# Kernel optimization log

Measured on AMD Instinct MI355X. Metric: run time of the kernel, lower is better.

The kernel has to match this reference:

```python
import math
import jax, jax.numpy as jnp
from jax import lax
import numpy as np

THETA = 10.0      # spiking threshold
TAU_SR = 10.0     # SRM (psp) alpha-kernel time constant
TAU_REF = 1.0     # refractory alpha-kernel time constant
SCALE_REF = 2.0   # refractory scale (kernel = -scaleRef*theta*alpha)
TAU_RHO = 1.0     # surrogate-gradient width
TS = 1.0          # simulation time step


def _alpha_filter_scan(x, tau, extra_input_fn=None):
    """Causal convolution along last (time) axis with alpha kernel
    k[n] = (n*Ts/tau) * exp(1 - n*Ts/tau)  (k[0] = 0),
    implemented exactly as a 2-state linear recurrence.
    x: [N, C, T] -> out: [N, C, T]."""
    d = jnp.float32(math.exp(-TS / tau))
    c = jnp.float32(math.e * TS / tau)
    xT = jnp.moveaxis(x, -1, 0)  # [T, N, C]

    def step(carry, xt):
        p, a = carry
        a = d * (a + p)          # alpha response from inputs up to t-1
        p = d * p + xt           # pure exponential state
        return (p, a), a * c

    z = jnp.zeros_like(xT[0])
    _, out = lax.scan(step, (z, z), xT)
    return jnp.moveaxis(out, 0, -1)


def psp(x):
    return _alpha_filter_scan(x, TAU_SR)


@jax.custom_vjp
def spike_fn(v):
    # Heaviside threshold on (membrane - theta)
    return (v >= 0).astype(v.dtype)

def _spike_fwd(v):
    return spike_fn(v), v

def _spike_bwd(v, g):
    # SLAYER surrogate gradient: exponential pdf around threshold
    grad = (1.0 / TAU_RHO) * jnp.exp(-jnp.abs(v) / TAU_RHO)
    return (g * grad,)

spike_fn.defvjp(_spike_fwd, _spike_bwd)


def spike_layer(u_in):
    """Threshold-and-refract over time. u_in: [N, C, T] psp potentials.
    Refractory response = -scaleRef*theta * alpha_{tauRef}(past spikes)."""
    d = jnp.float32(math.exp(-TS / TAU_REF))
    c = jnp.float32(math.e * TS / TAU_REF)
    ref_scale = jnp.float32(-SCALE_REF * THETA)
    uT = jnp.moveaxis(u_in, -1, 0)  # [T, N, C]

    def step(carry, ut):
        p, a = carry
        a = d * (a + p)                      # refractory potential at t
        u = ut + c * a                       # membrane potential
        s = spike_fn(u - THETA)              # spikes (0/1)
        p = d * p + ref_scale * s            # inject refractory impulse
        return (p, a), s

    z = jnp.zeros_like(uT[0])
    _, s = lax.scan(step, (z, z), uT)
    return jnp.moveaxis(s, 0, -1)


def setup_inputs() -> dict:
    key = jax.random.key(0)
    k1, k2, k3 = jax.random.split(key, 3)
    N, I, H, O, T = 64, 256, 1024, 18, 500
    # Bernoulli(0.1) input spikes
    spike_input = (jax.random.uniform(k1, (N, I, T)) < 0.1).astype(jnp.float32)
    W1 = jax.random.normal(k2, (H, I), dtype=jnp.float32) * (1.0 / math.sqrt(I))
    W2 = jax.random.normal(k3, (O, H), dtype=jnp.float32) * (1.0 / math.sqrt(H))
    return {"spike_input": spike_input, "W1": W1, "W2": W2}


def reference(spike_input, W1, W2):
    # layer 1: dense (per-timestep linear) -> psp -> spike
    y1 = jnp.einsum('nit,hi->nht', spike_input, W1)
    s1 = spike_layer(psp(y1))
    # layer 2
    y2 = jnp.einsum('nht,oh->not', s1, W2)
    s2 = spike_layer(psp(y2))
    return s2
```

## Files before the change

kernel.cpp:

```cpp
#include <hip/hip_runtime.h>


#define NN 64
#define II 256
#define HH 1024
#define OO 18
#define TT 500

#define D_SR 0.9048374180359595f
#define C_SR 0.27182818284590454f
#define D_RF 0.36787944117144233f
#define C_RF 2.718281828459045f
#define THETA 10.0f
#define REFS (-20.0f)

typedef _Float16 f16;
typedef _Float16 f16x8 __attribute__((ext_vector_type(8)));
typedef float f32x4 __attribute__((ext_vector_type(4)));

__device__ __forceinline__ void gl2lds16(const void* g, void* l) {
    __builtin_amdgcn_global_load_lds(
        (const __attribute__((address_space(1))) void*)g,
        (__attribute__((address_space(3))) void*)l, 16, 0, 0);
}

__launch_bounds__(256)
__global__ void prep_all(const float* __restrict__ X, const float* __restrict__ W1,
                         const float* __restrict__ W2, f16* __restrict__ Xb,
                         f16* __restrict__ W1h, f16* __restrict__ W1l,
                         f16* __restrict__ W2h, f16* __restrict__ W2l) {
    __shared__ float tile[64][65];
    const int b = blockIdx.x;
    const int tid = threadIdx.x;

    if (b < 2048) {
        const int t0 = (b & 7) * 64, i0 = ((b >> 3) & 3) * 64, n = b >> 5;
        const int tx = tid & 63, q = tid >> 6;
        const float* Xn = X + (size_t)n * II * TT;
#pragma unroll 4
        for (int j = 0; j < 16; ++j) {
            int il = j * 4 + q;
            int t = t0 + tx;
            tile[il][tx] = (t < TT) ? Xn[(size_t)(i0 + il) * TT + t] : 0.f;
        }
        __syncthreads();
#pragma unroll 4
        for (int j = 0; j < 16; ++j) {
            int tl = j * 4 + q;
            int t = t0 + tl;
            if (t < TT)
                Xb[((size_t)n * TT + t) * II + i0 + tx] = (f16)tile[tx][tl];
        }
    } else if (b < 3072) {
        int idx = (b - 2048) * 256 + tid;
        float w = W1[idx];
        f16 h = (f16)w;
        f16 l = (f16)(w - (float)h);
        W1h[idx] = h;
        W1l[idx] = l;
    } else {
        int idx = (b - 3072) * 256 + tid;
        int o = idx >> 10;
        float w = (o < OO) ? W2[idx] : 0.f;
        f16 h = (f16)w;
        f16 l = (f16)(w - (float)h);
        W2h[idx] = h;
        W2l[idx] = l;
    }
}

__launch_bounds__(512)
__global__ void gemm1_scan1(const f16* __restrict__ Xb, const f16* __restrict__ Wh,
                            const f16* __restrict__ Wl, f16* __restrict__ S1) {
    __shared__ __align__(16) char smem[3 * 24576];
    float* yb = (float*)smem;

    const int tid = threadIdx.x;
    const int wave = tid >> 6, lane = tid & 63;

    const int f = blockIdx.y * 8 + blockIdx.x;
    const int x = f & 7, g = f >> 3;
    const int n = x * 8 + (g & 7);
    const int ht = g >> 3;
    const int h0g = ht * 128;

    const int rbl = wave * 16 + (lane >> 2);
    const int koff = (((lane & 3) ^ ((lane >> 3) & 3))) * 8;
    const f16* gBh0 = Wh + (size_t)(h0g + rbl) * II + koff;
    const f16* gBl0 = Wl + (size_t)(h0g + rbl) * II + koff;

    const int wm = wave & 1, wn = wave >> 1;
    const int fr = lane & 15, kq = lane >> 4;
    const int kz = (kq ^ ((fr >> 1) & 3)) * 8;

    float p1 = 0.f, a1 = 0.f, p2 = 0.f, a2 = 0.f;

    for (int c = 0; c < 4; ++c) {
        const int t0 = c * 128;
        const int TCe = (TT - t0 < 128) ? (TT - t0) : 128;

        int r0 = rbl; if (r0 > TCe - 1) r0 = TCe - 1;
        const f16* gA0 = Xb + ((size_t)n * TT + t0 + r0) * II + koff;

        auto stage = [&](int kk2, int b) {
            f16* As_b = (f16*)(smem + b * 24576);
            f16* Bh_b = As_b + 4096;
            f16* Bl_b = As_b + 8192;
            const int ko = kk2 * 32;
            gl2lds16(gA0 + ko, As_b + wave * 512);
            gl2lds16(gBh0 + ko, Bh_b + wave * 512);
            gl2lds16(gBl0 + ko, Bl_b + wave * 512);
        };

        stage(0, 0);
        stage(1, 1);

        f32x4 acc[4][2] = {};
#pragma unroll
        for (int kk = 0; kk < 8; ++kk) {
            if (kk < 7) asm volatile("s_waitcnt vmcnt(3)" ::: "memory");
            else        asm volatile("s_waitcnt vmcnt(0)" ::: "memory");
            __builtin_amdgcn_s_barrier();
            __builtin_amdgcn_sched_barrier(0);
            if (kk < 6) stage(kk + 2, (kk + 2) % 3);

            const f16* As_b = (const f16*)(smem + (kk % 3) * 24576);
            const f16* Bh_b = As_b + 4096;
            const f16* Bl_b = As_b + 8192;

            f16x8 av[4], bhv[2], blv[2];
#pragma unroll
            for (int i = 0; i < 4; ++i)
                av[i] = *(const f16x8*)(As_b + (wm * 64 + i * 16 + fr) * 32 + kz);
#pragma unroll
            for (int j = 0; j < 2; ++j) {
                bhv[j] = *(const f16x8*)(Bh_b + (wn * 32 + j * 16 + fr) * 32 + kz);
                blv[j] = *(const f16x8*)(Bl_b + (wn * 32 + j * 16 + fr) * 32 + kz);
            }
            __builtin_amdgcn_s_setprio(1);
#pragma unroll
            for (int i = 0; i < 4; ++i)
#pragma unroll
                for (int j = 0; j < 2; ++j) {
                    acc[i][j] = __builtin_amdgcn_mfma_f32_16x16x32_f16(av[i], bhv[j], acc[i][j], 0, 0, 0);
                    acc[i][j] = __builtin_amdgcn_mfma_f32_16x16x32_f16(av[i], blv[j], acc[i][j], 0, 0, 0);
                }
            __builtin_amdgcn_s_setprio(0);
        }
        __syncthreads();

#pragma unroll
        for (int i = 0; i < 4; ++i)
#pragma unroll
            for (int j = 0; j < 2; ++j) {
                int tr = wm * 64 + i * 16 + kq * 4;
                int hc = wn * 32 + j * 16 + fr;
#pragma unroll
                for (int r = 0; r < 4; ++r)
                    yb[(tr + r) * 132 + hc] = acc[i][j][r];
            }
        __syncthreads();

        if (tid < 128) {
            f16* sq = S1 + ((size_t)n * TT + t0) * HH + h0g + tid;
            float rb_[8];
#pragma unroll
            for (int j = 0; j < 8; ++j) rb_[j] = yb[j * 132 + tid];
            int t = 0;
            for (; t + 8 <= TCe; t += 8) {
#pragma unroll
                for (int j = 0; j < 8; ++j) {
                    float xv = rb_[j];
                    int tn = t + j + 8;
                    rb_[j] = (tn < TCe) ? yb[tn * 132 + tid] : 0.f;
                    a1 = D_SR * (a1 + p1);
                    p1 = D_SR * p1 + xv;
                    float ut = C_SR * a1;
                    a2 = D_RF * (a2 + p2);
                    float u = ut + C_RF * a2;
                    float s = (u >= THETA) ? 1.0f : 0.0f;
                    p2 = D_RF * p2 + REFS * s;
                    sq[(size_t)(t + j) * HH] = (f16)s;
                }
            }
            int rem = TCe - t;
#pragma unroll
            for (int j = 0; j < 8; ++j) {
                if (j < rem) {
                    float xv = rb_[j];
                    a1 = D_SR * (a1 + p1);
                    p1 = D_SR * p1 + xv;
                    float ut = C_SR * a1;
                    a2 = D_RF * (a2 + p2);
                    float u = ut + C_RF * a2;
                    float s = (u >= THETA) ? 1.0f : 0.0f;
                    p2 = D_RF * p2 + REFS * s;
                    sq[(size_t)(t + j) * HH] = (f16)s;
                }
            }
        }
        __syncthreads();
    }
}

__launch_bounds__(256)
__global__ void gemm2_mfma(const f16* __restrict__ S1, const f16* __restrict__ W2h,
                           const f16* __restrict__ W2l, float* __restrict__ Y2) {
    __shared__ __align__(16) f16 As[3][64 * 32];
    __shared__ __align__(16) f16 Bh[3][32 * 32];
    __shared__ __align__(16) f16 Bl[3][32 * 32];

    const int tid = threadIdx.x;
    const int wave = tid >> 6, lane = tid & 63;
    const int m0 = blockIdx.x * 64;
    const int fr = lane & 15, kq = lane >> 4;
    const int koff = (((lane & 3) ^ ((lane >> 3) & 3))) * 8;
    const int kz = (kq ^ ((fr >> 1) & 3)) * 8;

    const f16* gA = S1 + (size_t)(m0 + wave * 16 + (lane >> 2)) * HH + koff;
    const f16* gB = (wave < 2 ? W2h : W2l) + (size_t)((wave & 1) * 16 + (lane >> 2)) * HH + koff;

    auto stage = [&](int kk2, int b) {
        const int ko = kk2 * 32;
        gl2lds16(gA + ko, &As[b][wave * 512]);
        gl2lds16(gB + ko, (wave < 2 ? &Bh[b][0] : &Bl[b][0]) + (wave & 1) * 512);
    };

    stage(0, 0);
    stage(1, 1);

    f32x4 acc[2] = {};
#pragma unroll
    for (int kk = 0; kk < HH / 32; ++kk) {
        if (kk < HH / 32 - 1) asm volatile("s_waitcnt vmcnt(2)" ::: "memory");
        else                  asm volatile("s_waitcnt vmcnt(0)" ::: "memory");
        __builtin_amdgcn_s_barrier();
        __builtin_amdgcn_sched_barrier(0);
        if (kk < HH / 32 - 2) stage(kk + 2, (kk + 2) % 3);
        const int b = kk % 3;

        f16x8 a, bh[2], bl[2];
        a = *(const f16x8*)(&As[b][(wave * 16 + fr) * 32 + kz]);
#pragma unroll
        for (int j = 0; j < 2; ++j) {
            bh[j] = *(const f16x8*)(&Bh[b][(j * 16 + fr) * 32 + kz]);
            bl[j] = *(const f16x8*)(&Bl[b][(j * 16 + fr) * 32 + kz]);
        }
        __builtin_amdgcn_s_setprio(1);
#pragma unroll
        for (int j = 0; j < 2; ++j) {
            acc[j] = __builtin_amdgcn_mfma_f32_16x16x32_f16(a, bh[j], acc[j], 0, 0, 0);
            acc[j] = __builtin_amdgcn_mfma_f32_16x16x32_f16(a, bl[j], acc[j], 0, 0, 0);
        }
        __builtin_amdgcn_s_setprio(0);
    }

#pragma unroll
    for (int j = 0; j < 2; ++j) {
        int rbase = m0 + wave * 16 + kq * 4;
        int cc = j * 16 + fr;
        float* p = Y2 + (size_t)rbase * 32 + cc;
#pragma unroll
        for (int r = 0; r < 4; ++r)
            p[(size_t)r * 32] = acc[j][r];
    }
}

__launch_bounds__(256)
__global__ void scan2_k(const float* __restrict__ Y2, float* __restrict__ Out) {
    __shared__ float yc[TT * 32];
    __shared__ float sb[OO * TT];
    const int n = blockIdx.x, tid = threadIdx.x;

    const float4* src = (const float4*)(Y2 + (size_t)n * TT * 32);
    float4* dst = (float4*)yc;
    for (int i = tid; i < TT * 8; i += 256) dst[i] = src[i];
    __syncthreads();

    if (tid < 32) {
        float p1 = 0.f, a1 = 0.f, p2 = 0.f, a2 = 0.f;
        float rb_[8];
#pragma unroll
        for (int j = 0; j < 8; ++j) rb_[j] = yc[j * 32 + tid];
        int t = 0;
        for (; t + 8 <= TT; t += 8) {
#pragma unroll
            for (int j = 0; j < 8; ++j) {
                float xv = rb_[j];
                int tn = t + j + 8;
                rb_[j] = (tn < TT) ? yc[tn * 32 + tid] : 0.f;
                a1 = D_SR * (a1 + p1);
                p1 = D_SR * p1 + xv;
                float ut = C_SR * a1;
                a2 = D_RF * (a2 + p2);
                float u = ut + C_RF * a2;
                float s = (u >= THETA) ? 1.0f : 0.0f;
                p2 = D_RF * p2 + REFS * s;
                if (tid < OO) sb[tid * TT + t + j] = s;
            }
        }
#pragma unroll
        for (int j = 0; j < 8; ++j) {
            if (t + j < TT) {
                float xv = rb_[j];
                a1 = D_SR * (a1 + p1);
                p1 = D_SR * p1 + xv;
                float ut = C_SR * a1;
                a2 = D_RF * (a2 + p2);
                float u = ut + C_RF * a2;
                float s = (u >= THETA) ? 1.0f : 0.0f;
                p2 = D_RF * p2 + REFS * s;
                if (tid < OO) sb[tid * TT + t + j] = s;
            }
        }
    }
    __syncthreads();

    float* on = Out + (size_t)n * OO * TT;
    for (int e = tid; e < OO * TT; e += 256) on[e] = sb[e];
}

extern "C" void kernel_launch(void* const* d_in, const int* in_sizes, int n_in,
                              void* d_out, int out_size, void* d_ws, size_t ws_size,
                              hipStream_t stream) {
    const float* X  = (const float*)d_in[0];
    const float* W1 = (const float*)d_in[1];
    const float* W2 = (const float*)d_in[2];
    float* out = (float*)d_out;

    const size_t s_s1 = (size_t)NN * TT * HH * 2;
    const size_t s_Xb = (size_t)NN * TT * II * 2;
    const size_t s_W  = (size_t)HH * II * 2;
    const size_t s_W2 = (size_t)32 * HH * 2;

    char* w = (char*)d_ws;
    f16*   s1b = (f16*)w;  w += s_s1;
    f16*   Xb  = (f16*)w;  w += s_Xb;
    f16*   W1h = (f16*)w;  w += s_W;
    f16*   W1l = (f16*)w;  w += s_W;
    f16*   W2h = (f16*)w;  w += s_W2;
    f16*   W2l = (f16*)w;  w += s_W2;
    float* y2  = (float*)w;

    prep_all<<<3200, 256, 0, stream>>>(X, W1, W2, Xb, W1h, W1l, W2h, W2l);

    gemm1_scan1<<<dim3(8, NN), 512, 0, stream>>>(Xb, W1h, W1l, s1b);

    gemm2_mfma<<<(NN * TT) / 64, 256, 0, stream>>>(s1b, W2h, W2l, y2);
    scan2_k<<<NN, 256, 0, stream>>>(y2, out);
}
```

Before: 187.4 us.

## Overlap scan of previous time chunk with GEMM of next chunk in gemm1

Restructures gemm1_scan1 so the serial psp/spike scan for chunk c-1 runs interleaved with the MFMA k-loop of chunk c, using two ping-pong LDS regions. The per-timestep scalar f16 spike stores are replaced by spike bits packed into LDS and flushed as coalesced 16-byte vector stores by all threads. The k-loop pipeline drops from triple to double buffering with plain __syncthreads, setprio is removed, and occupancy is hinted at 2 blocks per CU. LDS use grows, which may in practice prevent the second resident block, and the scan still runs on only 128 threads while the other waves sit at barriers.

After: 201.1 us. 7.3% more time.

```diff
diff --git a/kernel.cpp b/kernel.cpp
--- a/kernel.cpp
+++ b/kernel.cpp
@@ -17,6 +17,7 @@
 typedef _Float16 f16;
 typedef _Float16 f16x8 __attribute__((ext_vector_type(8)));
 typedef float f32x4 __attribute__((ext_vector_type(4)));
+typedef unsigned int uint;
 
 __device__ __forceinline__ void gl2lds16(const void* g, void* l) {
     __builtin_amdgcn_global_load_lds(
@@ -69,11 +70,11 @@
     }
 }
 
-__launch_bounds__(512)
+__launch_bounds__(512, 2)
 __global__ void gemm1_scan1(const f16* __restrict__ Xb, const f16* __restrict__ Wh,
                             const f16* __restrict__ Wl, f16* __restrict__ S1) {
-    __shared__ __align__(16) char smem[3 * 24576];
-    float* yb = (float*)smem;
+    __shared__ __align__(16) char smem_[2][67584];
+    __shared__ uint sbits[4][128];
 
     const int tid = threadIdx.x;
     const int wave = tid >> 6, lane = tid & 63;
@@ -95,36 +96,52 @@
 
     float p1 = 0.f, a1 = 0.f, p2 = 0.f, a2 = 0.f;
 
+    auto mkA = [&](int c) -> const f16* {
+        int r = c * 128 + rbl;
+        if (r > TT - 1) r = TT - 1;
+        return Xb + ((size_t)n * TT + r) * II + koff;
+    };
+    auto stage = [&](const f16* gA0c, int kk2, int b, char* regp) {
+        f16* As_b = (f16*)(regp + b * 24576);
+        const int ko = kk2 * 32;
+        gl2lds16(gA0c + ko, As_b + wave * 512);
+        gl2lds16(gBh0 + ko, As_b + 4096 + wave * 512);
+        gl2lds16(gBl0 + ko, As_b + 8192 + wave * 512);
+    };
+    auto flush = [&](int tc0, int TC) {
+#pragma unroll
+        for (int v = 0; v < 4; ++v) {
+            int slot = v * 512 + tid;
+            int t = slot >> 4, h8 = slot & 15;
+            if (t < TC) {
+                int wsel = t >> 5, bit = t & 31;
+                f16x8 vv;
+#pragma unroll
+                for (int e = 0; e < 8; ++e) {
+                    uint wv = sbits[wsel][h8 * 8 + e];
+                    vv[e] = (f16)(float)((wv >> bit) & 1u);
+                }
+                *(f16x8*)(S1 + ((size_t)n * TT + tc0 + t) * HH + h0g + h8 * 8) = vv;
+            }
+        }
+    };
+
+    const f16* gA0c = mkA(0);
+    stage(gA0c, 0, 0, smem_[0]);
+
     for (int c = 0; c < 4; ++c) {
-        const int t0 = c * 128;
-        const int TCe = (TT - t0 < 128) ? (TT - t0) : 128;
-
-        int r0 = rbl; if (r0 > TCe - 1) r0 = TCe - 1;
-        const f16* gA0 = Xb + ((size_t)n * TT + t0 + r0) * II + koff;
-
-        auto stage = [&](int kk2, int b) {
-            f16* As_b = (f16*)(smem + b * 24576);
-            f16* Bh_b = As_b + 4096;
-            f16* Bl_b = As_b + 8192;
-            const int ko = kk2 * 32;
-            gl2lds16(gA0 + ko, As_b + wave * 512);
-            gl2lds16(gBh0 + ko, Bh_b + wave * 512);
-            gl2lds16(gBl0 + ko, Bl_b + wave * 512);
-        };
-
-        stage(0, 0);
-        stage(1, 1);
+        char* reg = smem_[c & 1];
+        const float* ybp = (const float*)smem_[(c + 1) & 1];
+        float* yb = (float*)reg;
 
         f32x4 acc[4][2] = {};
+        uint tmpw = 0;
 #pragma unroll
         for (int kk = 0; kk < 8; ++kk) {
-            if (kk < 7) asm volatile("s_waitcnt vmcnt(3)" ::: "memory");
-            else        asm volatile("s_waitcnt vmcnt(0)" ::: "memory");
-            __builtin_amdgcn_s_barrier();
-            __builtin_amdgcn_sched_barrier(0);
-            if (kk < 6) stage(kk + 2, (kk + 2) % 3);
-
-            const f16* As_b = (const f16*)(smem + (kk % 3) * 24576);
+            __syncthreads();
+            if (kk < 7) stage(gA0c, kk + 1, (kk + 1) & 1, reg);
+
+            const f16* As_b = (const f16*)(reg + (kk & 1) * 24576);
             const f16* Bh_b = As_b + 4096;
             const f16* Bl_b = As_b + 8192;
 
@@ -137,7 +154,6 @@
                 bhv[j] = *(const f16x8*)(Bh_b + (wn * 32 + j * 16 + fr) * 32 + kz);
                 blv[j] = *(const f16x8*)(Bl_b + (wn * 32 + j * 16 + fr) * 32 + kz);
             }
-            __builtin_amdgcn_s_setprio(1);
 #pragma unroll
             for (int i = 0; i < 4; ++i)
 #pragma unroll
@@ -145,61 +161,77 @@
                     acc[i][j] = __builtin_amdgcn_mfma_f32_16x16x32_f16(av[i], bhv[j], acc[i][j], 0, 0, 0);
                     acc[i][j] = __builtin_amdgcn_mfma_f32_16x16x32_f16(av[i], blv[j], acc[i][j], 0, 0, 0);
                 }
-            __builtin_amdgcn_s_setprio(0);
-        }
-        __syncthreads();
-
-#pragma unroll
-        for (int i = 0; i < 4; ++i)
-#pragma unroll
-            for (int j = 0; j < 2; ++j) {
-                int tr = wm * 64 + i * 16 + kq * 4;
-                int hc = wn * 32 + j * 16 + fr;
-#pragma unroll
-                for (int r = 0; r < 4; ++r)
-                    yb[(tr + r) * 132 + hc] = acc[i][j][r];
-            }
-        __syncthreads();
-
-        if (tid < 128) {
-            f16* sq = S1 + ((size_t)n * TT + t0) * HH + h0g + tid;
-            float rb_[8];
-#pragma unroll
-            for (int j = 0; j < 8; ++j) rb_[j] = yb[j * 132 + tid];
-            int t = 0;
-            for (; t + 8 <= TCe; t += 8) {
-#pragma unroll
-                for (int j = 0; j < 8; ++j) {
-                    float xv = rb_[j];
-                    int tn = t + j + 8;
-                    rb_[j] = (tn < TCe) ? yb[tn * 132 + tid] : 0.f;
+
+            if (c > 0 && tid < 128) {
+                float xv[16];
+#pragma unroll
+                for (int j = 0; j < 16; ++j)
+                    xv[j] = ybp[(kk * 16 + j) * 132 + tid];
+                uint mbits = 0;
+#pragma unroll
+                for (int j = 0; j < 16; ++j) {
                     a1 = D_SR * (a1 + p1);
-                    p1 = D_SR * p1 + xv;
+                    p1 = D_SR * p1 + xv[j];
                     float ut = C_SR * a1;
                     a2 = D_RF * (a2 + p2);
                     float u = ut + C_RF * a2;
                     float s = (u >= THETA) ? 1.0f : 0.0f;
                     p2 = D_RF * p2 + REFS * s;
-                    sq[(size_t)(t + j) * HH] = (f16)s;
+                    mbits |= (u >= THETA ? 1u : 0u) << j;
                 }
-            }
-            int rem = TCe - t;
-#pragma unroll
-            for (int j = 0; j < 8; ++j) {
-                if (j < rem) {
-                    float xv = rb_[j];
-                    a1 = D_SR * (a1 + p1);
-                    p1 = D_SR * p1 + xv;
-                    float ut = C_SR * a1;
-                    a2 = D_RF * (a2 + p2);
-                    float u = ut + C_RF * a2;
-                    float s = (u >= THETA) ? 1.0f : 0.0f;
-                    p2 = D_RF * p2 + REFS * s;
-                    sq[(size_t)(t + j) * HH] = (f16)s;
+                if ((kk & 1) == 0) tmpw = mbits;
+                else sbits[kk >> 1][tid] = tmpw | (mbits << 16);
+            }
+        }
+        __syncthreads();
+
+        if (c < 3) {
+            gA0c = mkA(c + 1);
+            stage(gA0c, 0, 0, smem_[(c + 1) & 1]);
+        }
+        if (c > 0) flush((c - 1) * 128, 128);
+
+#pragma unroll
+        for (int i = 0; i < 4; ++i)
+#pragma unroll
+            for (int j = 0; j < 2; ++j) {
+                int tr = wm * 64 + i * 16 + kq * 4;
+                int hc = wn * 32 + j * 16 + fr;
+#pragma unroll
+                for (int r = 0; r < 4; ++r)
+                    yb[(tr + r) * 132 + hc] = acc[i][j][r];
+            }
+        __syncthreads();
+    }
+
+    {
+        const float* ybp = (const float*)smem_[1];
+        if (tid < 128) {
+            uint tmpw = 0;
+#pragma unroll
+            for (int kk = 0; kk < 8; ++kk) {
+                uint mbits = 0;
+#pragma unroll
+                for (int j = 0; j < 16; ++j) {
+                    int t = kk * 16 + j;
+                    if (t < TT - 384) {
+                        float xv = ybp[t * 132 + tid];
+                        a1 = D_SR * (a1 + p1);
+                        p1 = D_SR * p1 + xv;
+                        float ut = C_SR * a1;
+                        a2 = D_RF * (a2 + p2);
+                        float u = ut + C_RF * a2;
+                        float s = (u >= THETA) ? 1.0f : 0.0f;
+                        p2 = D_RF * p2 + REFS * s;
+                        mbits |= (u >= THETA ? 1u : 0u) << j;
+                    }
                 }
+                if ((kk & 1) == 0) tmpw = mbits;
+                else sbits[kk >> 1][tid] = tmpw | (mbits << 16);
             }
         }
         __syncthreads();
+        flush(384, TT - 384);
     }
 }
 
```

## Bit-pack layer-1 spikes via wave ballot and expand bits in gemm2

Applied to the files above, without the earlier changes.

The scan in gemm1_scan1 now stores each layer-1 spike as a bit in a 64-bit ballot mask instead of one f16 per neuron. This shrinks the intermediate S1 buffer by 16x in both write and read traffic. gemm2 drops its LDS triple-buffered pipeline: it loads each row's 1024 bits into registers, expands bytes into f16 vectors for the MFMA, and reads W2 directly from global memory. That adds bit-unpacking ALU work and unstaged, unpipelined weight loads in exchange for the much smaller activation traffic.

Result: slower. 210.2 us (+12.2%).

```diff
diff --git a/kernel.cpp b/kernel.cpp
--- a/kernel.cpp
+++ b/kernel.cpp
@@ -17,6 +17,8 @@
 typedef _Float16 f16;
 typedef _Float16 f16x8 __attribute__((ext_vector_type(8)));
 typedef float f32x4 __attribute__((ext_vector_type(4)));
+typedef unsigned int uint;
+typedef unsigned long long u64;
 
 __device__ __forceinline__ void gl2lds16(const void* g, void* l) {
     __builtin_amdgcn_global_load_lds(
@@ -71,7 +73,7 @@
 
 __launch_bounds__(512)
 __global__ void gemm1_scan1(const f16* __restrict__ Xb, const f16* __restrict__ Wh,
-                            const f16* __restrict__ Wl, f16* __restrict__ S1) {
+                            const f16* __restrict__ Wl, u64* __restrict__ Sb) {
     __shared__ __align__(16) char smem[3 * 24576];
     float* yb = (float*)smem;
 
@@ -162,7 +164,7 @@
         __syncthreads();
 
         if (tid < 128) {
-            f16* sq = S1 + ((size_t)n * TT + t0) * HH + h0g + tid;
+            u64* sq = Sb + ((size_t)n * TT + t0) * 16 + ht * 2 + wave;
             float rb_[8];
 #pragma unroll
             for (int j = 0; j < 8; ++j) rb_[j] = yb[j * 132 + tid];
@@ -180,7 +182,8 @@
                     float u = ut + C_RF * a2;
                     float s = (u >= THETA) ? 1.0f : 0.0f;
                     p2 = D_RF * p2 + REFS * s;
-                    sq[(size_t)(t + j) * HH] = (f16)s;
+                    u64 m = __ballot(u >= THETA);
+                    if (lane == 0) sq[(size_t)(t + j) * 16] = m;
                 }
             }
             int rem = TCe - t;
@@ -195,7 +198,8 @@
                     float u = ut + C_RF * a2;
                     float s = (u >= THETA) ? 1.0f : 0.0f;
                     p2 = D_RF * p2 + REFS * s;
-                    sq[(size_t)(t + j) * HH] = (f16)s;
+                    u64 m = __ballot(u >= THETA);
+                    if (lane == 0) sq[(size_t)(t + j) * 16] = m;
                 }
             }
         }
@@ -204,55 +208,47 @@
 }
 
 __launch_bounds__(256)
-__global__ void gemm2_mfma(const f16* __restrict__ S1, const f16* __restrict__ W2h,
+__global__ void gemm2_mfma(const uint* __restrict__ Ab, const f16* __restrict__ W2h,
                            const f16* __restrict__ W2l, float* __restrict__ Y2) {
-    __shared__ __align__(16) f16 As[3][64 * 32];
-    __shared__ __align__(16) f16 Bh[3][32 * 32];
-    __shared__ __align__(16) f16 Bl[3][32 * 32];
-
     const int tid = threadIdx.x;
     const int wave = tid >> 6, lane = tid & 63;
     const int m0 = blockIdx.x * 64;
     const int fr = lane & 15, kq = lane >> 4;
-    const int koff = (((lane & 3) ^ ((lane >> 3) & 3))) * 8;
-    const int kz = (kq ^ ((fr >> 1) & 3)) * 8;
-
-    const f16* gA = S1 + (size_t)(m0 + wave * 16 + (lane >> 2)) * HH + koff;
-    const f16* gB = (wave < 2 ? W2h : W2l) + (size_t)((wave & 1) * 16 + (lane >> 2)) * HH + koff;
-
-    auto stage = [&](int kk2, int b) {
-        const int ko = kk2 * 32;
-        gl2lds16(gA + ko, &As[b][wave * 512]);
-        gl2lds16(gB + ko, (wave < 2 ? &Bh[b][0] : &Bl[b][0]) + (wave & 1) * 512);
-    };
-
-    stage(0, 0);
-    stage(1, 1);
+
+    const int row = m0 + wave * 16 + fr;
+    const uint* arow = Ab + (size_t)row * 32;
+    const int sh = kq * 8;
+
+    const f16* bh0 = W2h + (size_t)fr * HH + kq * 8;
+    const f16* bh1 = bh0 + (size_t)16 * HH;
+    const f16* bl0 = W2l + (size_t)fr * HH + kq * 8;
+    const f16* bl1 = bl0 + (size_t)16 * HH;
+
+    uint wrow[32];
+#pragma unroll
+    for (int q = 0; q < 8; ++q)
+        *(uint4*)&wrow[q * 4] = *(const uint4*)(arow + q * 4);
 
     f32x4 acc[2] = {};
 #pragma unroll
     for (int kk = 0; kk < HH / 32; ++kk) {
-        if (kk < HH / 32 - 1) asm volatile("s_waitcnt vmcnt(2)" ::: "memory");
-        else                  asm volatile("s_waitcnt vmcnt(0)" ::: "memory");
-        __builtin_amdgcn_s_barrier();
-        __builtin_amdgcn_sched_barrier(0);
-        if (kk < HH / 32 - 2) stage(kk + 2, (kk + 2) % 3);
-        const int b = kk % 3;
-
-        f16x8 a, bh[2], bl[2];
-        a = *(const f16x8*)(&As[b][(wave * 16 + fr) * 32 + kz]);
-#pragma unroll
-        for (int j = 0; j < 2; ++j) {
-            bh[j] = *(const f16x8*)(&Bh[b][(j * 16 + fr) * 32 + kz]);
-            bl[j] = *(const f16x8*)(&Bl[b][(j * 16 + fr) * 32 + kz]);
-        }
-        __builtin_amdgcn_s_setprio(1);
-#pragma unroll
-        for (int j = 0; j < 2; ++j) {
-            acc[j] = __builtin_amdgcn_mfma_f32_16x16x32_f16(a, bh[j], acc[j], 0, 0, 0);
-            acc[j] = __builtin_amdgcn_mfma_f32_16x16x32_f16(a, bl[j], acc[j], 0, 0, 0);
-        }
-        __builtin_amdgcn_s_setprio(0);
+        const uint byte = (wrow[kk] >> sh) & 0xFFu;
+        f16x8 a;
+#pragma unroll
+        for (int e = 0; e < 8; ++e)
+            a[e] = (byte & (1u << e)) ? (f16)1.0f : (f16)0.0f;
+
+        const int ko = kk * 32;
+        f16x8 bh[2], bl[2];
+        bh[0] = *(const f16x8*)(bh0 + ko);
+        bh[1] = *(const f16x8*)(bh1 + ko);
+        bl[0] = *(const f16x8*)(bl0 + ko);
+        bl[1] = *(const f16x8*)(bl1 + ko);
+
+        acc[0] = __builtin_amdgcn_mfma_f32_16x16x32_f16(a, bh[0], acc[0], 0, 0, 0);
+        acc[0] = __builtin_amdgcn_mfma_f32_16x16x32_f16(a, bl[0], acc[0], 0, 0, 0);
+        acc[1] = __builtin_amdgcn_mfma_f32_16x16x32_f16(a, bh[1], acc[1], 0, 0, 0);
+        acc[1] = __builtin_amdgcn_mfma_f32_16x16x32_f16(a, bl[1], acc[1], 0, 0, 0);
     }
 
 #pragma unroll
@@ -328,13 +324,13 @@
     const float* W2 = (const float*)d_in[2];
     float* out = (float*)d_out;
 
-    const size_t s_s1 = (size_t)NN * TT * HH * 2;
+    const size_t s_sb = (size_t)NN * TT * 16 * 8;
     const size_t s_Xb = (size_t)NN * TT * II * 2;
     const size_t s_W  = (size_t)HH * II * 2;
     const size_t s_W2 = (size_t)32 * HH * 2;
 
     char* w = (char*)d_ws;
-    f16*   s1b = (f16*)w;  w += s_s1;
+    u64*   sbb = (u64*)w;  w += s_sb;
     f16*   Xb  = (f16*)w;  w += s_Xb;
     f16*   W1h = (f16*)w;  w += s_W;
     f16*   W1l = (f16*)w;  w += s_W;
@@ -344,8 +340,8 @@
 
     prep_all<<<3200, 256, 0, stream>>>(X, W1, W2, Xb, W1h, W1l, W2h, W2l);
 
-    gemm1_scan1<<<dim3(8, NN), 512, 0, stream>>>(Xb, W1h, W1l, s1b);
-
-    gemm2_mfma<<<(NN * TT) / 64, 256, 0, stream>>>(s1b, W2h, W2l, y2);
+    gemm1_scan1<<<dim3(8, NN), 512, 0, stream>>>(Xb, W1h, W1l, sbb);
+
+    gemm2_mfma<<<(NN * TT) / 64, 256, 0, stream>>>((const uint*)sbb, W2h, W2l, y2);
     scan2_k<<<NN, 256, 0, stream>>>(y2, out);
 }
```
